# Kernel optimization log

Hardware: AMD Instinct MI355X
Metric: run time of the kernel (lower is better)

## Reference

```python
import jax, jax.numpy as jnp
import numpy as np

H1, H2 = 96, 64


def _lstm_scan(x_tbd, Wih, Whh, bih, bhh, hidden):
    """x_tbd: [T, B, D]. Returns (outputs [T, B, hidden], final h [B, hidden]).
    PyTorch gate order: i, f, g, o."""
    T, B, _ = x_tbd.shape
    b = bih + bhh  # fuse biases once
    # precompute input projections for all timesteps: [T, B, 4H]
    x_proj = jnp.einsum('tbd,hd->tbh', x_tbd, Wih) + b

    def step(carry, xp):
        h, c = carry
        gates = xp + h @ Whh.T  # [B, 4H]
        i, f, g, o = jnp.split(gates, 4, axis=-1)
        i = jax.nn.sigmoid(i)
        f = jax.nn.sigmoid(f)
        g = jnp.tanh(g)
        o = jax.nn.sigmoid(o)
        c = f * c + i * g
        h = o * jnp.tanh(c)
        return (h, c), h

    h0 = jnp.zeros((B, hidden), x_tbd.dtype)
    c0 = jnp.zeros((B, hidden), x_tbd.dtype)
    (hT, _), hs = jax.lax.scan(step, (h0, c0), x_proj)
    return hs, hT


def setup_inputs() -> dict:
    key = jax.random.key(0)
    ks = jax.random.split(key, 16)
    B, T, D, HOR = 4096, 336, 8, 24
    s1 = 1.0 / np.sqrt(H1)
    s2 = 1.0 / np.sqrt(H2)
    u = lambda k, shape, s: jax.random.uniform(k, shape, jnp.float32, -s, s)
    return {
        'x': jax.random.normal(ks[0], (B, T, D), jnp.float32),
        'Wih1': u(ks[1], (4 * H1, D), s1),
        'Whh1': u(ks[2], (4 * H1, H1), s1),
        'bih1': u(ks[3], (4 * H1,), s1),
        'bhh1': u(ks[4], (4 * H1,), s1),
        'Wih2': u(ks[5], (4 * H2, H1), s2),
        'Whh2': u(ks[6], (4 * H2, H2), s2),
        'bih2': u(ks[7], (4 * H2,), s2),
        'bhh2': u(ks[8], (4 * H2,), s2),
        'fc1_w': u(ks[9], (64, H2), s2),
        'fc1_b': u(ks[10], (64,), s2),
        'fco_w': u(ks[11], (HOR, 64), s2),
        'fco_b': u(ks[12], (HOR,), s2),
    }


def reference(x, Wih1, Whh1, bih1, bhh1, Wih2, Whh2, bih2, bhh2,
              fc1_w, fc1_b, fco_w, fco_b):
    # dropout layers are identity in eval mode
    x_tbd = jnp.transpose(x, (1, 0, 2))  # [T, B, D]
    hs1, _ = _lstm_scan(x_tbd, Wih1, Whh1, bih1, bhh1, H1)  # [T, B, 96]
    _, hT2 = _lstm_scan(hs1, Wih2, Whh2, bih2, bhh2, H2)    # [B, 64] = last timestep
    h = jax.nn.relu(hT2 @ fc1_w.T + fc1_b)
    return h @ fco_w.T + fco_b  # [B, horizon]
```

## Files before the change

kernel.cpp:

```cpp
#include <hip/hip_runtime.h>
#include <hip/hip_bf16.h>

namespace {

constexpr int T_LEN = 336;
constexpr int D_IN  = 8;
constexpr int NH1   = 96;
constexpr int NH2   = 64;
constexpr int HOR   = 24;
constexpr int BM    = 16;
constexpr int KPAD  = 200;


typedef __attribute__((ext_vector_type(8))) short short8;
typedef __attribute__((ext_vector_type(4))) float f32x4;

constexpr float LOG2E = 1.4426950408889634f;

__device__ inline unsigned short f2b(float f) {
  union { float f; unsigned u; } v; v.f = f;
  unsigned r = v.u + 0x7fffu + ((v.u >> 16) & 1u);
  return (unsigned short)(r >> 16);
}

__device__ inline short8 pack8s(float4 p0, float4 p1, float s) {
  short8 f;
  f[0]=(short)f2b(p0.x*s); f[1]=(short)f2b(p0.y*s); f[2]=(short)f2b(p0.z*s); f[3]=(short)f2b(p0.w*s);
  f[4]=(short)f2b(p1.x*s); f[5]=(short)f2b(p1.y*s); f[6]=(short)f2b(p1.z*s); f[7]=(short)f2b(p1.w*s);
  return f;
}

__device__ inline unsigned cvt_pk_bf16(float a, float b) {
  unsigned r;
  asm("v_cvt_pk_bf16_f32 %0, %1, %2" : "=v"(r) : "v"(a), "v"(b));
  return r;
}

#if __has_builtin(__builtin_amdgcn_exp2f)
__device__ inline float exp2_(float x) { return __builtin_amdgcn_exp2f(x); }
#else
__device__ inline float exp2_(float x) { float r; asm("v_exp_f32 %0, %1" : "=v"(r) : "v"(x)); return r; }
#endif

__device__ inline float cell_update(const f32x4 acc, float& c) {
  const float Ei = exp2_(acc[0]);
  const float Ef = exp2_(acc[1]);
  const float Eg = exp2_(acc[2]);
  const float Eo = exp2_(acc[3]);
  const float Di = 1.0f + Ei, Df = 1.0f + Ef, Dg = 1.0f + Eg, Dq = 1.0f + Eo;
  const float Pig = Di * Dg;
  const float R   = __builtin_amdgcn_rcpf(Pig * Df);
  const float fv  = Pig * R;
  const float ig  = (1.0f - Eg) * (Df * R);
  c = fmaf(fv, c, ig);
  const float yc = fminf(c * (-2.0f * LOG2E), 60.0f);
  const float Ec = exp2_(yc);
  const float R2 = __builtin_amdgcn_rcpf(Dq * (1.0f + Ec));
  return (1.0f - Ec) * R2;
}

__global__ __launch_bounds__(1024, 4) void lstm_forecaster(
    const float* __restrict__ x,
    const float* __restrict__ Wih1, const float* __restrict__ Whh1,
    const float* __restrict__ bih1, const float* __restrict__ bhh1,
    const float* __restrict__ Wih2, const float* __restrict__ Whh2,
    const float* __restrict__ bih2, const float* __restrict__ bhh2,
    const float* __restrict__ fc1w, const float* __restrict__ fc1b,
    const float* __restrict__ fcow, const float* __restrict__ fcob,
    float* __restrict__ out)
{
  __shared__ unsigned short Hc[2][BM * KPAD];
  __shared__ float h2f[BM][NH2];
  __shared__ float fcb[BM][NH2 + 4];

  const int tid  = threadIdx.x;
  const int w    = tid >> 6;
  const int l    = tid & 63;
  const int lrow = l & 15;
  const int lgrp = l >> 4;
  const int b0   = blockIdx.x * BM;
  const bool isL1 = (w < 8);
  const int  wv   = isL1 ? w : (w - 8);

  const float* xrow = x + (size_t)(b0 + lrow) * (T_LEN * D_IN) + lgrp * 2;
  float2 xv = make_float2(0.0f, 0.0f);
  if (w == 8) xv = *(const float2*)(xrow);

  for (int i = tid; i < 2 * BM * KPAD; i += 1024) ((unsigned short*)Hc)[i] = 0;

  short8 af[12];
  float  bs[12];
  if (isL1) {
    #pragma unroll
    for (int mt = 0; mt < 3; ++mt) {
      const int gate = lrow & 3;
      const float gs = (gate == 2) ? (-2.0f * LOG2E) : (-LOG2E);
      const int cell = wv * 12 + mt * 4 + (lrow >> 2);
      const int wrow = NH1 * gate + cell;
      #pragma unroll
      for (int kt = 0; kt < 4; ++kt) {
        const int kb = kt * 32 + lgrp * 8;
        if (kb < NH1) {
          af[mt*4+kt] = pack8s(*(const float4*)(Whh1 + wrow * NH1 + kb),
                               *(const float4*)(Whh1 + wrow * NH1 + kb + 4), gs);
        } else if (kb == NH1) {
          af[mt*4+kt] = pack8s(*(const float4*)(Wih1 + wrow * D_IN),
                               *(const float4*)(Wih1 + wrow * D_IN + 4), gs);
        } else {
          short8 z;
          #pragma unroll
          for (int e = 0; e < 8; ++e) z[e] = 0;
          af[mt*4+kt] = z;
        }
      }
      const int bcell = wv * 12 + mt * 4 + lgrp;
      #pragma unroll
      for (int r = 0; r < 4; ++r) {
        const float bsc = (r == 2) ? (-2.0f * LOG2E) : (-LOG2E);
        bs[mt*4+r] = bsc * (bih1[NH1 * r + bcell] + bhh1[NH1 * r + bcell]);
      }
    }
  } else {
    #pragma unroll
    for (int mt = 0; mt < 2; ++mt) {
      const int gate = lrow & 3;
      const float gs = (gate == 2) ? (-2.0f * LOG2E) : (-LOG2E);
      const int cell = wv * 8 + mt * 4 + (lrow >> 2);
      const int wrow = NH2 * gate + cell;
      #pragma unroll
      for (int kt = 0; kt < 5; ++kt) {
        const int kb = kt * 32 + lgrp * 8;
        if (kb < NH2) {
          af[mt*5+kt] = pack8s(*(const float4*)(Whh2 + wrow * NH2 + kb),
                               *(const float4*)(Whh2 + wrow * NH2 + kb + 4), gs);
        } else {
          af[mt*5+kt] = pack8s(*(const float4*)(Wih2 + wrow * NH1 + (kb - NH2)),
                               *(const float4*)(Wih2 + wrow * NH1 + (kb - NH2) + 4), gs);
        }
      }
      const int bcell = wv * 8 + mt * 4 + lgrp;
      #pragma unroll
      for (int r = 0; r < 4; ++r) {
        const float bsc = (r == 2) ? (-2.0f * LOG2E) : (-LOG2E);
        bs[mt*4+r] = bsc * (bih2[NH2 * r + bcell] + bhh2[NH2 * r + bcell]);
      }
    }
  }

  __syncthreads();
  if (w == 8) {
    *(unsigned*)&Hc[1][lrow * KPAD + 160 + lgrp * 2] = cvt_pk_bf16(xv.x, xv.y);
  }
  __syncthreads();

  float c[3] = {0.0f, 0.0f, 0.0f};
  const int rbo = lrow * KPAD;

  {
    if (w == 8) {
      xv = *(const float2*)(xrow + D_IN);
      *(unsigned*)&Hc[0][rbo + 160 + lgrp * 2] = cvt_pk_bf16(xv.x, xv.y);
    }
    if (isL1) {
      short8 bf[4];
      #pragma unroll
      for (int kt = 0; kt < 4; ++kt)
        bf[kt] = *(const short8*)(&Hc[1][rbo + 64 + lgrp * 8 + kt * 32]);
      #pragma unroll
      for (int mt = 0; mt < 3; ++mt) {
        f32x4 acc = { bs[mt*4+0], bs[mt*4+1], bs[mt*4+2], bs[mt*4+3] };
        #pragma unroll
        for (int kt = 0; kt < 4; ++kt)
          acc = __builtin_amdgcn_mfma_f32_16x16x32_bf16(af[mt*4+kt], bf[kt], acc, 0, 0, 0);
        Hc[0][rbo + 64 + wv * 12 + mt * 4 + lgrp] = f2b(cell_update(acc, c[mt]));
      }
    }
    __syncthreads();
  }

  #pragma unroll 2
  for (int p = 0; p < T_LEN - 1; ++p) {
    const unsigned short* RB = &Hc[p & 1][0];
    unsigned short*       WB = &Hc[(p & 1) ^ 1][0];

    if (isL1) {
      short8 bf[4];
      #pragma unroll
      for (int kt = 0; kt < 4; ++kt)
        bf[kt] = *(const short8*)(RB + rbo + 64 + lgrp * 8 + kt * 32);
      float h1v[3];
      #pragma unroll
      for (int mt = 0; mt < 3; ++mt) {
        f32x4 acc = { bs[mt*4+0], bs[mt*4+1], bs[mt*4+2], bs[mt*4+3] };
        #pragma unroll
        for (int kt = 0; kt < 4; ++kt)
          acc = __builtin_amdgcn_mfma_f32_16x16x32_bf16(af[mt*4+kt], bf[kt], acc, 0, 0, 0);
        h1v[mt] = cell_update(acc, c[mt]);
      }
      const unsigned pk01 = cvt_pk_bf16(h1v[0], h1v[1]);
      const unsigned pk2  = cvt_pk_bf16(h1v[2], h1v[2]);
      WB[rbo + 64 + wv * 12 + 0 + lgrp] = (unsigned short)pk01;
      WB[rbo + 64 + wv * 12 + 4 + lgrp] = (unsigned short)(pk01 >> 16);
      WB[rbo + 64 + wv * 12 + 8 + lgrp] = (unsigned short)pk2;
    } else {
      if (w == 8 && p + 2 < T_LEN)
        xv = *(const float2*)(xrow + (p + 2) * D_IN);
      short8 bf[5];
      #pragma unroll
      for (int kt = 0; kt < 5; ++kt)
        bf[kt] = *(const short8*)(RB + rbo + lgrp * 8 + kt * 32);
      float h2v[2];
      #pragma unroll
      for (int mt = 0; mt < 2; ++mt) {
        f32x4 acc = { bs[mt*4+0], bs[mt*4+1], bs[mt*4+2], bs[mt*4+3] };
        #pragma unroll
        for (int kt = 0; kt < 5; ++kt)
          acc = __builtin_amdgcn_mfma_f32_16x16x32_bf16(af[mt*5+kt], bf[kt], acc, 0, 0, 0);
        h2v[mt] = cell_update(acc, c[mt]);
      }
      const unsigned pk = cvt_pk_bf16(h2v[0], h2v[1]);
      WB[rbo + wv * 8 + 0 + lgrp] = (unsigned short)pk;
      WB[rbo + wv * 8 + 4 + lgrp] = (unsigned short)(pk >> 16);
      if (w == 8 && p + 2 < T_LEN)
        *(unsigned*)&WB[rbo + 160 + lgrp * 2] = cvt_pk_bf16(xv.x, xv.y);
    }
    __syncthreads();
  }

  if (!isL1) {
    const unsigned short* RB = &Hc[(T_LEN - 1) & 1][0];
    short8 bf[5];
    #pragma unroll
    for (int kt = 0; kt < 5; ++kt)
      bf[kt] = *(const short8*)(RB + rbo + lgrp * 8 + kt * 32);
    #pragma unroll
    for (int mt = 0; mt < 2; ++mt) {
      f32x4 acc = { bs[mt*4+0], bs[mt*4+1], bs[mt*4+2], bs[mt*4+3] };
      #pragma unroll
      for (int kt = 0; kt < 5; ++kt)
        acc = __builtin_amdgcn_mfma_f32_16x16x32_bf16(af[mt*5+kt], bf[kt], acc, 0, 0, 0);
      h2f[lrow][wv * 8 + mt * 4 + lgrp] = cell_update(acc, c[mt]);
    }
  }
  __syncthreads();

  {
    const int col = tid >> 6;
    const int j   = tid & 63;
    float s = fc1b[j];
    const float* wr = fc1w + j * NH2;
    #pragma unroll 8
    for (int k = 0; k < NH2; ++k) s += h2f[col][k] * wr[k];
    fcb[col][j] = fmaxf(s, 0.0f);
  }
  __syncthreads();
  if (tid < BM * HOR) {
    const int col = tid / HOR;
    const int oc  = tid - col * HOR;
    float s = fcob[oc];
    const float* wr = fcow + oc * NH2;
    #pragma unroll 8
    for (int k = 0; k < NH2; ++k) s += fcb[col][k] * wr[k];
    out[(size_t)(b0 + col) * HOR + oc] = s;
  }
}

}

extern "C" void kernel_launch(void* const* d_in, const int* in_sizes, int n_in,
                              void* d_out, int out_size, void* d_ws, size_t ws_size,
                              hipStream_t stream) {
  const float* x    = (const float*)d_in[0];
  const float* Wih1 = (const float*)d_in[1];
  const float* Whh1 = (const float*)d_in[2];
  const float* bih1 = (const float*)d_in[3];
  const float* bhh1 = (const float*)d_in[4];
  const float* Wih2 = (const float*)d_in[5];
  const float* Whh2 = (const float*)d_in[6];
  const float* bih2 = (const float*)d_in[7];
  const float* bhh2 = (const float*)d_in[8];
  const float* fc1w = (const float*)d_in[9];
  const float* fc1b = (const float*)d_in[10];
  const float* fcow = (const float*)d_in[11];
  const float* fcob = (const float*)d_in[12];
  float* out = (float*)d_out;

  const int Btot = in_sizes[0] / (T_LEN * D_IN);
  const int nblk = Btot / BM;

  lstm_forecaster<<<dim3(nblk), dim3(1024), 0, stream>>>(
      x, Wih1, Whh1, bih1, bhh1, Wih2, Whh2, bih2, bhh2,
      fc1w, fc1b, fcow, fcob, out);
}
```

Measured before the change: 304.1 us.

## Replace per-step block barriers with LDS counter flags between LSTM layer waves

Swaps the block-wide __syncthreads per timestep for producer/consumer counters in LDS. Layer-1 and layer-2 wavefronts now run decoupled pipelines, and a 4-deep layer-1 ring buffer lets layer 1 run up to three steps ahead of layer 2. Layer-1 wave 0 now streams x into the layer-1 buffer instead of wave 8. The goal is to stop the slower wave group from stalling the other every step, at the cost of spin-wait polling with s_sleep, atomic traffic, and more LDS.

```diff
diff --git a/kernel.cpp b/kernel.cpp
--- a/kernel.cpp
+++ b/kernel.cpp
@@ -9,7 +9,8 @@
 constexpr int NH2   = 64;
 constexpr int HOR   = 24;
 constexpr int BM    = 16;
-constexpr int KPAD  = 200;
+constexpr int S1    = 136;
+constexpr int S2    = 72;
 
 
 typedef __attribute__((ext_vector_type(8))) short short8;
@@ -39,7 +40,7 @@
 #if __has_builtin(__builtin_amdgcn_exp2f)
 __device__ inline float exp2_(float x) { return __builtin_amdgcn_exp2f(x); }
 #else
-__device__ inline float exp2_(float x) { float r; asm("v_exp_f32 %0, %1" : "=v"(r) : "v"(x)); return r; }
+__device__ inline float exp2_(float x) { return __builtin_exp2f(x); }
 #endif
 
 __device__ inline float cell_update(const f32x4 acc, float& c) {
@@ -59,6 +60,30 @@
   return (1.0f - Ec) * R2;
 }
 
+__device__ inline int lds_wait_ge(const int* cnt, int target) {
+  if (target <= 0) return 0;
+  int v = __hip_atomic_load(cnt, __ATOMIC_ACQUIRE, __HIP_MEMORY_SCOPE_WORKGROUP);
+  while (v < target) {
+    __builtin_amdgcn_s_sleep(1);
+    v = __hip_atomic_load(cnt, __ATOMIC_ACQUIRE, __HIP_MEMORY_SCOPE_WORKGROUP);
+  }
+  asm volatile("s_waitcnt lgkmcnt(0)" ::: "memory");
+  __builtin_amdgcn_sched_barrier(0);
+  return v;
+}
+
+__device__ inline void signal_done(int* cnt, bool lane0) {
+  __builtin_amdgcn_sched_barrier(0);
+  asm volatile("s_waitcnt lgkmcnt(0)" ::: "memory");
+  if (lane0) __hip_atomic_fetch_add(cnt, 1, __ATOMIC_RELEASE, __HIP_MEMORY_SCOPE_WORKGROUP);
+  __builtin_amdgcn_sched_barrier(0);
+}
+
+__device__ inline int launder(int ofs, int gv) {
+  asm("" : "+v"(ofs) : "v"(gv));
+  return ofs;
+}
+
 __global__ __launch_bounds__(1024, 4) void lstm_forecaster(
     const float* __restrict__ x,
     const float* __restrict__ Wih1, const float* __restrict__ Whh1,
@@ -69,9 +94,11 @@
     const float* __restrict__ fcow, const float* __restrict__ fcob,
     float* __restrict__ out)
 {
-  __shared__ unsigned short Hc[2][BM * KPAD];
+  __shared__ unsigned short H1X[4][BM * S1];
+  __shared__ unsigned short H2b[2][BM * S2];
   __shared__ float h2f[BM][NH2];
   __shared__ float fcb[BM][NH2 + 4];
+  __shared__ int cnt[2];
 
   const int tid  = threadIdx.x;
   const int w    = tid >> 6;
@@ -83,10 +110,12 @@
   const int  wv   = isL1 ? w : (w - 8);
 
   const float* xrow = x + (size_t)(b0 + lrow) * (T_LEN * D_IN) + lgrp * 2;
-  float2 xv = make_float2(0.0f, 0.0f);
-  if (w == 8) xv = *(const float2*)(xrow);
-
-  for (int i = tid; i < 2 * BM * KPAD; i += 1024) ((unsigned short*)Hc)[i] = 0;
+  float2 x0v = make_float2(0.f, 0.f), xv = make_float2(0.f, 0.f);
+  if (w == 0) { x0v = *(const float2*)(xrow); xv = *(const float2*)(xrow + D_IN); }
+
+  for (int i = tid; i < 4 * BM * S1; i += 1024) ((unsigned short*)H1X)[i] = 0;
+  for (int i = tid; i < 2 * BM * S2; i += 1024) ((unsigned short*)H2b)[i] = 0;
+  if (tid == 0) { cnt[0] = 0; cnt[1] = 0; }
 
   short8 af[12];
   float  bs[12];
@@ -148,46 +177,31 @@
   }
 
   __syncthreads();
-  if (w == 8) {
-    *(unsigned*)&Hc[1][lrow * KPAD + 160 + lgrp * 2] = cvt_pk_bf16(xv.x, xv.y);
-  }
+  if (w == 0)
+    *(unsigned*)&H1X[3][lrow * S1 + 96 + lgrp * 2] = cvt_pk_bf16(x0v.x, x0v.y);
   __syncthreads();
 
-  float c[3] = {0.0f, 0.0f, 0.0f};
-  const int rbo = lrow * KPAD;
-
-  {
-    if (w == 8) {
-      xv = *(const float2*)(xrow + D_IN);
-      *(unsigned*)&Hc[0][rbo + 160 + lgrp * 2] = cvt_pk_bf16(xv.x, xv.y);
-    }
-    if (isL1) {
+  const int rb1 = lrow * S1;
+  const int rb2 = lrow * S2;
+
+  if (isL1) {
+    float c[3] = {0.f, 0.f, 0.f};
+    for (int i = 0; i < T_LEN; ++i) {
+      const int v0 = lds_wait_ge(&cnt[0], 8 * i);
+      const int v1 = lds_wait_ge(&cnt[1], 8 * (i - 3));
+      const int gv = v0 + v1;
+
+      float2 xnext;
+      if (w == 0 && i + 2 < T_LEN) xnext = *(const float2*)(xrow + (i + 2) * D_IN);
+
+      const unsigned short* RB = &H1X[(i + 3) & 3][launder(rb1, gv)];
+      unsigned short*       WB = &H1X[i & 3][launder(rb1, gv)];
+
       short8 bf[4];
       #pragma unroll
       for (int kt = 0; kt < 4; ++kt)
-        bf[kt] = *(const short8*)(&Hc[1][rbo + 64 + lgrp * 8 + kt * 32]);
-      #pragma unroll
-      for (int mt = 0; mt < 3; ++mt) {
-        f32x4 acc = { bs[mt*4+0], bs[mt*4+1], bs[mt*4+2], bs[mt*4+3] };
-        #pragma unroll
-        for (int kt = 0; kt < 4; ++kt)
-          acc = __builtin_amdgcn_mfma_f32_16x16x32_bf16(af[mt*4+kt], bf[kt], acc, 0, 0, 0);
-        Hc[0][rbo + 64 + wv * 12 + mt * 4 + lgrp] = f2b(cell_update(acc, c[mt]));
-      }
-    }
-    __syncthreads();
-  }
-
-  #pragma unroll 2
-  for (int p = 0; p < T_LEN - 1; ++p) {
-    const unsigned short* RB = &Hc[p & 1][0];
-    unsigned short*       WB = &Hc[(p & 1) ^ 1][0];
-
-    if (isL1) {
-      short8 bf[4];
-      #pragma unroll
-      for (int kt = 0; kt < 4; ++kt)
-        bf[kt] = *(const short8*)(RB + rbo + 64 + lgrp * 8 + kt * 32);
+        bf[kt] = *(const short8*)(RB + lgrp * 8 + kt * 32);
+
       float h1v[3];
       #pragma unroll
       for (int mt = 0; mt < 3; ++mt) {
@@ -199,16 +213,34 @@
       }
       const unsigned pk01 = cvt_pk_bf16(h1v[0], h1v[1]);
       const unsigned pk2  = cvt_pk_bf16(h1v[2], h1v[2]);
-      WB[rbo + 64 + wv * 12 + 0 + lgrp] = (unsigned short)pk01;
-      WB[rbo + 64 + wv * 12 + 4 + lgrp] = (unsigned short)(pk01 >> 16);
-      WB[rbo + 64 + wv * 12 + 8 + lgrp] = (unsigned short)pk2;
-    } else {
-      if (w == 8 && p + 2 < T_LEN)
-        xv = *(const float2*)(xrow + (p + 2) * D_IN);
+      WB[wv * 12 + 0 + lgrp] = (unsigned short)pk01;
+      WB[wv * 12 + 4 + lgrp] = (unsigned short)(pk01 >> 16);
+      WB[wv * 12 + 8 + lgrp] = (unsigned short)pk2;
+      if (w == 0 && i + 1 < T_LEN) {
+        *(unsigned*)(WB + 96 + lgrp * 2) = cvt_pk_bf16(xv.x, xv.y);
+        xv = xnext;
+      }
+      signal_done(&cnt[0], l == 0);
+    }
+  } else {
+    float c[2] = {0.f, 0.f};
+    for (int q = 0; q < T_LEN; ++q) {
+      const int v1 = lds_wait_ge(&cnt[1], 8 * q);
+      const int v0 = lds_wait_ge(&cnt[0], 8 * (q + 1));
+      const int gv = v0 + v1;
+
+      const unsigned short* RH2 = &H2b[(q + 1) & 1][launder(rb2, gv)];
+      const unsigned short* RH1 = &H1X[q & 3][launder(rb1, gv)];
+      unsigned short*       WB  = &H2b[q & 1][launder(rb2, gv)];
+
       short8 bf[5];
       #pragma unroll
-      for (int kt = 0; kt < 5; ++kt)
-        bf[kt] = *(const short8*)(RB + rbo + lgrp * 8 + kt * 32);
+      for (int kt = 0; kt < 2; ++kt)
+        bf[kt] = *(const short8*)(RH2 + lgrp * 8 + kt * 32);
+      #pragma unroll
+      for (int kt = 0; kt < 3; ++kt)
+        bf[2 + kt] = *(const short8*)(RH1 + lgrp * 8 + kt * 32);
+
       float h2v[2];
       #pragma unroll
       for (int mt = 0; mt < 2; ++mt) {
@@ -218,30 +250,18 @@
           acc = __builtin_amdgcn_mfma_f32_16x16x32_bf16(af[mt*5+kt], bf[kt], acc, 0, 0, 0);
         h2v[mt] = cell_update(acc, c[mt]);
       }
-      const unsigned pk = cvt_pk_bf16(h2v[0], h2v[1]);
-      WB[rbo + wv * 8 + 0 + lgrp] = (unsigned short)pk;
-      WB[rbo + wv * 8 + 4 + lgrp] = (unsigned short)(pk >> 16);
-      if (w == 8 && p + 2 < T_LEN)
-        *(unsigned*)&WB[rbo + 160 + lgrp * 2] = cvt_pk_bf16(xv.x, xv.y);
+      if (q < T_LEN - 1) {
+        const unsigned pk = cvt_pk_bf16(h2v[0], h2v[1]);
+        WB[wv * 8 + 0 + lgrp] = (unsigned short)pk;
+        WB[wv * 8 + 4 + lgrp] = (unsigned short)(pk >> 16);
+        signal_done(&cnt[1], l == 0);
+      } else {
+        h2f[lrow][wv * 8 + 0 + lgrp] = h2v[0];
+        h2f[lrow][wv * 8 + 4 + lgrp] = h2v[1];
+      }
     }
-    __syncthreads();
-  }
-
-  if (!isL1) {
-    const unsigned short* RB = &Hc[(T_LEN - 1) & 1][0];
-    short8 bf[5];
-    #pragma unroll
-    for (int kt = 0; kt < 5; ++kt)
-      bf[kt] = *(const short8*)(RB + rbo + lgrp * 8 + kt * 32);
-    #pragma unroll
-    for (int mt = 0; mt < 2; ++mt) {
-      f32x4 acc = { bs[mt*4+0], bs[mt*4+1], bs[mt*4+2], bs[mt*4+3] };
-      #pragma unroll
-      for (int kt = 0; kt < 5; ++kt)
-        acc = __builtin_amdgcn_mfma_f32_16x16x32_bf16(af[mt*5+kt], bf[kt], acc, 0, 0, 0);
-      h2f[lrow][wv * 8 + mt * 4 + lgrp] = cell_update(acc, c[mt]);
-    }
-  }
+  }
+
   __syncthreads();
 
   {
```

After: 358.3 us. 17.8% more time.
